# Performance work log

Hardware: AMD Instinct MI355X
Metric: run time of the kernel (lower is better)

## Reference

```python
import jax, jax.numpy as jnp
import numpy as np

B, S = 64, 1000
ENC, DEC = 512, 512


def setup_inputs() -> dict:
    key = jax.random.key(0)
    k1, k2, k3, k4, k5 = jax.random.split(key, 5)
    hidden = jax.random.normal(k1, (B, DEC), dtype=jnp.float32)
    encoder_outputs = jax.random.normal(k2, (B, S, 2 * ENC), dtype=jnp.float32)
    # attn: Linear(enc_hidden_dim*2 + dec_hidden_dim -> dec_hidden_dim)
    fan_in = 2 * ENC + DEC
    bound = 1.0 / np.sqrt(fan_in)
    attn_w = jax.random.uniform(k3, (fan_in, DEC), minval=-bound, maxval=bound, dtype=jnp.float32)
    attn_b = jax.random.uniform(k4, (DEC,), minval=-bound, maxval=bound, dtype=jnp.float32)
    v = jax.random.uniform(k5, (DEC,), dtype=jnp.float32)  # torch.rand -> U[0,1)
    return {"hidden": hidden, "encoder_outputs": encoder_outputs,
            "attn_w": attn_w, "attn_b": attn_b, "v": v}


def reference(hidden, encoder_outputs, attn_w, attn_b, v):
    # hidden: [B, D], encoder_outputs: [B, S, 2E]
    S_len = encoder_outputs.shape[1]
    h_rep = jnp.broadcast_to(hidden[:, None, :], (hidden.shape[0], S_len, hidden.shape[1]))
    cat = jnp.concatenate([h_rep, encoder_outputs], axis=2)          # [B, S, D+2E]
    energy = jnp.tanh(cat @ attn_w + attn_b)                          # [B, S, D]
    attention = jnp.einsum('bsd,d->bs', energy, v)                    # [B, S]
    return jax.nn.softmax(attention, axis=1)
```

## Files before the change

### kernel.cpp

```cpp
#include <hip/hip_runtime.h>
#include <hip/hip_bf16.h>

typedef __attribute__((ext_vector_type(8))) short short8;
typedef __attribute__((ext_vector_type(4))) float float4v;

__device__ inline unsigned short f2bf(float f) {
    union { float f; unsigned int i; } c; c.f = f;
    unsigned int r = c.i + 0x7FFFu + ((c.i >> 16) & 1u);
    return (unsigned short)(r >> 16);
}

__global__ void k_transpose(const float* __restrict__ W,
                            unsigned short* __restrict__ Wt) {
    int idx = blockIdx.x * 256 + threadIdx.x;
    int d  = idx & 511;
    int kg = idx >> 9;
    short8 v;
#pragma unroll
    for (int j = 0; j < 8; j++)
        v[j] = (short)f2bf(W[(size_t)(512 + kg * 8 + j) * 512 + d]);
    *(short8*)(Wt + (size_t)d * 1024 + kg * 8) = v;
}

__global__ void k_hb(const float* __restrict__ hidden,
                     const float* __restrict__ W,
                     const float* __restrict__ bias,
                     float* __restrict__ hb) {
    int b = blockIdx.y, dg = blockIdx.x, tid = threadIdx.x;
    int d = dg * 128 + tid;
    __shared__ float h[512];
    for (int k = tid; k < 512; k += 128) h[k] = hidden[b * 512 + k];
    __syncthreads();
    float a = 0.f;
#pragma unroll 16
    for (int k = 0; k < 512; k++)
        a += h[k] * W[(size_t)k * 512 + d];
    hb[b * 512 + d] = a + bias[d];
}

__launch_bounds__(512, 2)
__global__ void k_main(const float* __restrict__ enc,
                       const unsigned short* __restrict__ Wt,
                       const float* __restrict__ hb,
                       const float* __restrict__ vvec,
                       float* __restrict__ att) {
    const int b    = blockIdx.y;
    const int s0   = blockIdx.x * 64;
    const int tid  = threadIdx.x;
    const int wave = tid >> 6;
    const int lane = tid & 63;
    const int col  = lane & 15;
    const int quad = lane >> 4;

    __shared__ unsigned short As[2][64][72];
    __shared__ float red[8][64];

    const int r   = tid >> 3;
    const int seg = tid & 7;
    int s = s0 + r; if (s > 999) s = 999;
    const float* arow = enc + ((size_t)(b * 1000 + s) * 1024) + seg * 8;

    const unsigned short* bbase = Wt + (size_t)(wave * 64 + col) * 1024 + quad * 8;

    float4v acc[4][4];
#pragma unroll
    for (int mt = 0; mt < 4; mt++)
#pragma unroll
        for (int nt = 0; nt < 4; nt++)
            acc[mt][nt] = float4v{0.f, 0.f, 0.f, 0.f};

    short8  bf[2][8];
    float4v sp[2][2];

    {
        float4v a0 = *(const float4v*)(arow);
        float4v a1 = *(const float4v*)(arow + 4);
        short8 wv;
#pragma unroll
        for (int j = 0; j < 4; j++) { wv[j] = (short)f2bf(a0[j]); wv[j + 4] = (short)f2bf(a1[j]); }
        *(short8*)&As[0][r][seg * 8] = wv;
    }
    sp[0][0] = *(const float4v*)(arow + 64);
    sp[0][1] = *(const float4v*)(arow + 68);
#pragma unroll
    for (int nt = 0; nt < 4; nt++)
#pragma unroll
        for (int ks = 0; ks < 2; ks++)
            bf[0][nt * 2 + ks] = *(const short8*)(bbase + (size_t)nt * 16384 + ks * 32);
    __syncthreads();

#pragma unroll
    for (int c = 0; c < 16; c++) {
        const int cur = c & 1, nxt = cur ^ 1;

        if (c < 15) {
#pragma unroll
            for (int nt = 0; nt < 4; nt++)
#pragma unroll
                for (int ks = 0; ks < 2; ks++)
                    bf[nxt][nt * 2 + ks] =
                        *(const short8*)(bbase + (size_t)nt * 16384 + (c + 1) * 64 + ks * 32);
        }
        if (c < 14) {
            sp[nxt][0] = *(const float4v*)(arow + (c + 2) * 64);
            sp[nxt][1] = *(const float4v*)(arow + (c + 2) * 64 + 4);
        }

        short8 af[2][4];
#pragma unroll
        for (int ks = 0; ks < 2; ks++)
#pragma unroll
            for (int mt = 0; mt < 4; mt++)
                af[ks][mt] = *(const short8*)&As[cur][mt * 16 + col][ks * 32 + quad * 8];

#pragma unroll
        for (int ks = 0; ks < 2; ks++)
#pragma unroll
            for (int mt = 0; mt < 4; mt++)
#pragma unroll
                for (int nt = 0; nt < 4; nt++)
                    acc[mt][nt] = __builtin_amdgcn_mfma_f32_16x16x32_bf16(
                        af[ks][mt], bf[cur][nt * 2 + ks], acc[mt][nt], 0, 0, 0);

        if (c < 15) {
            short8 wv;
#pragma unroll
            for (int j = 0; j < 4; j++) {
                wv[j]     = (short)f2bf(sp[cur][0][j]);
                wv[j + 4] = (short)f2bf(sp[cur][1][j]);
            }
            *(short8*)&As[nxt][r][seg * 8] = wv;
        }
        __syncthreads();
    }

    float vv[4], hbv[4];
#pragma unroll
    for (int nt = 0; nt < 4; nt++) {
        int d = wave * 64 + nt * 16 + col;
        vv[nt]  = vvec[d];
        hbv[nt] = hb[b * 512 + d];
    }
    float rs[4][4];
#pragma unroll
    for (int mt = 0; mt < 4; mt++)
#pragma unroll
        for (int rg = 0; rg < 4; rg++) rs[mt][rg] = 0.f;

#pragma unroll
    for (int mt = 0; mt < 4; mt++)
#pragma unroll
        for (int nt = 0; nt < 4; nt++)
#pragma unroll
            for (int rg = 0; rg < 4; rg++) {
                float e = acc[mt][nt][rg] + hbv[nt];
                float t = 1.f - 2.f / (__expf(2.f * e) + 1.f);
                rs[mt][rg] += t * vv[nt];
            }

#pragma unroll
    for (int mt = 0; mt < 4; mt++)
#pragma unroll
        for (int rg = 0; rg < 4; rg++) {
            float x = rs[mt][rg];
            x += __shfl_xor(x, 1);
            x += __shfl_xor(x, 2);
            x += __shfl_xor(x, 4);
            x += __shfl_xor(x, 8);
            rs[mt][rg] = x;
        }

    if (col == 0) {
#pragma unroll
        for (int mt = 0; mt < 4; mt++)
#pragma unroll
            for (int rg = 0; rg < 4; rg++)
                red[wave][mt * 16 + quad * 4 + rg] = rs[mt][rg];
    }
    __syncthreads();
    if (tid < 64) {
        float sum = red[0][tid] + red[1][tid] + red[2][tid] + red[3][tid]
                  + red[4][tid] + red[5][tid] + red[6][tid] + red[7][tid];
        int ss = s0 + tid;
        if (ss < 1000) att[b * 1000 + ss] = sum;
    }
}

__global__ void k_softmax(const float* __restrict__ att,
                          float* __restrict__ out) {
    int b = blockIdx.x, tid = threadIdx.x;
    __shared__ float sm[4], ss[4];
    float x[4], mx = -1e30f;
#pragma unroll
    for (int i = 0; i < 4; i++) {
        int s = tid + 256 * i;
        x[i] = (s < 1000) ? att[b * 1000 + s] : -1e30f;
        mx = fmaxf(mx, x[i]);
    }
    for (int off = 1; off < 64; off <<= 1) mx = fmaxf(mx, __shfl_xor(mx, off));
    if ((tid & 63) == 0) sm[tid >> 6] = mx;
    __syncthreads();
    mx = fmaxf(fmaxf(sm[0], sm[1]), fmaxf(sm[2], sm[3]));

    float ex[4], se = 0.f;
#pragma unroll
    for (int i = 0; i < 4; i++) {
        ex[i] = __expf(x[i] - mx);
        if (tid + 256 * i >= 1000) ex[i] = 0.f;
        se += ex[i];
    }
    for (int off = 1; off < 64; off <<= 1) se += __shfl_xor(se, off);
    if ((tid & 63) == 0) ss[tid >> 6] = se;
    __syncthreads();
    se = ss[0] + ss[1] + ss[2] + ss[3];
    float inv = 1.f / se;
#pragma unroll
    for (int i = 0; i < 4; i++) {
        int s = tid + 256 * i;
        if (s < 1000) out[b * 1000 + s] = ex[i] * inv;
    }
}

extern "C" void kernel_launch(void* const* d_in, const int* in_sizes, int n_in,
                              void* d_out, int out_size, void* d_ws, size_t ws_size,
                              hipStream_t stream) {
    const float* hidden = (const float*)d_in[0];
    const float* enc    = (const float*)d_in[1];
    const float* attn_w = (const float*)d_in[2];
    const float* attn_b = (const float*)d_in[3];
    const float* v      = (const float*)d_in[4];
    float* out = (float*)d_out;

    char* ws = (char*)d_ws;
    unsigned short* Wt = (unsigned short*)ws;
    float* hb  = (float*)(ws + (1 << 20));
    float* att = (float*)(ws + (1 << 20) + (128 << 10));

    k_transpose<<<256, 256, 0, stream>>>(attn_w, Wt);
    k_hb<<<dim3(4, 64), 128, 0, stream>>>(hidden, attn_w, attn_b, hb);
    k_main<<<dim3(16, 64), 512, 0, stream>>>(enc, Wt, hb, v, att);
    k_softmax<<<64, 256, 0, stream>>>(att, out);
}
```

Measured before the change: 487.2 us.

## Drop register double-buffering in main GEMM to raise occupancy

```diff
diff --git a/kernel.cpp b/kernel.cpp
--- a/kernel.cpp
+++ b/kernel.cpp
@@ -38,7 +38,7 @@
     hb[b * 512 + d] = a + bias[d];
 }
 
-__launch_bounds__(512, 2)
+__launch_bounds__(512, 4)
 __global__ void k_main(const float* __restrict__ enc,
                        const unsigned short* __restrict__ Wt,
                        const float* __restrict__ hb,
@@ -69,9 +69,6 @@
         for (int nt = 0; nt < 4; nt++)
             acc[mt][nt] = float4v{0.f, 0.f, 0.f, 0.f};
 
-    short8  bf[2][8];
-    float4v sp[2][2];
-
     {
         float4v a0 = *(const float4v*)(arow);
         float4v a1 = *(const float4v*)(arow + 4);
@@ -80,54 +77,40 @@
         for (int j = 0; j < 4; j++) { wv[j] = (short)f2bf(a0[j]); wv[j + 4] = (short)f2bf(a1[j]); }
         *(short8*)&As[0][r][seg * 8] = wv;
     }
-    sp[0][0] = *(const float4v*)(arow + 64);
-    sp[0][1] = *(const float4v*)(arow + 68);
-#pragma unroll
-    for (int nt = 0; nt < 4; nt++)
-#pragma unroll
-        for (int ks = 0; ks < 2; ks++)
-            bf[0][nt * 2 + ks] = *(const short8*)(bbase + (size_t)nt * 16384 + ks * 32);
     __syncthreads();
 
 #pragma unroll
     for (int c = 0; c < 16; c++) {
         const int cur = c & 1, nxt = cur ^ 1;
 
+        float4v sp0, sp1;
         if (c < 15) {
+            sp0 = *(const float4v*)(arow + (c + 1) * 64);
+            sp1 = *(const float4v*)(arow + (c + 1) * 64 + 4);
+        }
+
+#pragma unroll
+        for (int ks = 0; ks < 2; ks++) {
+            short8 bf[4];
 #pragma unroll
             for (int nt = 0; nt < 4; nt++)
-#pragma unroll
-                for (int ks = 0; ks < 2; ks++)
-                    bf[nxt][nt * 2 + ks] =
-                        *(const short8*)(bbase + (size_t)nt * 16384 + (c + 1) * 64 + ks * 32);
-        }
-        if (c < 14) {
-            sp[nxt][0] = *(const float4v*)(arow + (c + 2) * 64);
-            sp[nxt][1] = *(const float4v*)(arow + (c + 2) * 64 + 4);
-        }
-
-        short8 af[2][4];
-#pragma unroll
-        for (int ks = 0; ks < 2; ks++)
-#pragma unroll
-            for (int mt = 0; mt < 4; mt++)
-                af[ks][mt] = *(const short8*)&As[cur][mt * 16 + col][ks * 32 + quad * 8];
-
-#pragma unroll
-        for (int ks = 0; ks < 2; ks++)
-#pragma unroll
-            for (int mt = 0; mt < 4; mt++)
+                bf[nt] = *(const short8*)(bbase + (size_t)nt * 16384 + c * 64 + ks * 32);
+#pragma unroll
+            for (int mt = 0; mt < 4; mt++) {
+                short8 af = *(const short8*)&As[cur][mt * 16 + col][ks * 32 + quad * 8];
 #pragma unroll
                 for (int nt = 0; nt < 4; nt++)
                     acc[mt][nt] = __builtin_amdgcn_mfma_f32_16x16x32_bf16(
-                        af[ks][mt], bf[cur][nt * 2 + ks], acc[mt][nt], 0, 0, 0);
+                        af, bf[nt], acc[mt][nt], 0, 0, 0);
+            }
+        }
 
         if (c < 15) {
             short8 wv;
 #pragma unroll
             for (int j = 0; j < 4; j++) {
-                wv[j]     = (short)f2bf(sp[cur][0][j]);
-                wv[j + 4] = (short)f2bf(sp[cur][1][j]);
+                wv[j]     = (short)f2bf(sp0[j]);
+                wv[j + 4] = (short)f2bf(sp1[j]);
             }
             *(short8*)&As[nxt][r][seg * 8] = wv;
         }
```

Result: no change. 495.1 us (+1.6%).
